# Kernel optimization log

Measured on AMD Instinct MI355X. Metric: run time of the kernel, lower is better.

Reference implementation:

```python
import jax, jax.numpy as jnp
import numpy as np

HEADS = 8
HIDDEN = 512
SEQ = 1024
BATCH = 8
SCALE = 1.2
TOPK = round(0.05 * SEQ)  # 51, as in mode='stocastic'


def setup_inputs() -> dict:
    key = jax.random.key(0)
    ks = jax.random.split(key, 12)
    d = HIDDEN
    s = 0.02
    return {
        "Query_x": jax.random.normal(ks[0], (BATCH, SEQ, d), jnp.float32),
        "KeyandValue_x": jax.random.normal(ks[1], (BATCH, SEQ, d), jnp.float32),
        "Wq": jax.random.normal(ks[2], (d, d), jnp.float32) * s,
        "bq": jnp.zeros((d,), jnp.float32),
        "Wk": jax.random.normal(ks[3], (d, d), jnp.float32) * s,
        "bk": jnp.zeros((d,), jnp.float32),
        "Wv": jax.random.normal(ks[4], (d, d), jnp.float32) * s,
        "bv": jnp.zeros((d,), jnp.float32),
        "Wo": jax.random.normal(ks[5], (d, d), jnp.float32) * s,
        "bo": jnp.zeros((d,), jnp.float32),
        "randidx": jax.random.randint(ks[6], (round(0.1 * SEQ),), 0, SEQ, jnp.int32),
    }


def _split_heads(x, B, S):
    # torch: split last dim into heads chunks, cat along dim 0 -> [heads*B, S, dk]
    dk = HIDDEN // HEADS
    return x.reshape(B, S, HEADS, dk).transpose(2, 0, 1, 3).reshape(HEADS * B, S, dk)


def _merge_heads(x, B, S):
    dk = HIDDEN // HEADS
    return x.reshape(HEADS, B, S, dk).transpose(1, 2, 0, 3).reshape(B, S, HIDDEN)


def moderate_attention(a, randidx):
    # a: [N, S, L] softmaxed attention. Scale top-k + random columns by SCALE,
    # then renormalize rows. torch scatter_ writes a*SCALE gathered from the
    # pre-scatter tensor, so duplicate indices are idempotent -> boolean mask.
    N, S, L = a.shape
    _, idx = jax.lax.top_k(a, TOPK)                       # [N, S, k]
    rand_b = jnp.broadcast_to(randidx.astype(idx.dtype), (N, S, randidx.shape[0]))
    all_idx = jnp.concatenate([idx, rand_b], axis=-1)      # [N, S, k+r]
    n_ix = jnp.arange(N)[:, None, None]
    q_ix = jnp.arange(S)[None, :, None]
    sel = jnp.zeros(a.shape, bool).at[n_ix, q_ix, all_idx].set(True)
    a2 = jnp.where(sel, a * SCALE, a)
    return a2 / jnp.sum(a2, axis=-1, keepdims=True)


def reference(Query_x, KeyandValue_x, Wq, bq, Wk, bk, Wv, bv, Wo, bo, randidx):
    B, S, _ = Query_x.shape
    dk = HIDDEN // HEADS
    Q = _split_heads(Query_x @ Wq + bq, B, S)          # [H*B, S, dk]
    K = _split_heads(KeyandValue_x @ Wk + bk, B, S)
    V = _split_heads(KeyandValue_x @ Wv + bv, B, S)
    scores = jnp.einsum('nqd,nkd->nqk', Q, K) / jnp.sqrt(jnp.float32(dk))
    a = jax.nn.softmax(scores, axis=-1)
    a = moderate_attention(a, randidx)
    out = jnp.einsum('nqk,nkd->nqd', a, V)
    return _merge_heads(out, B, S) @ Wo + bo
```

## Files before the change

kernel.cpp:

```cpp
#include <hip/hip_runtime.h>
#include <stdint.h>

typedef unsigned short ushort_t;
typedef __bf16 bf16x8 __attribute__((ext_vector_type(8)));
typedef _Float16 f16x8v __attribute__((ext_vector_type(8)));
typedef __fp16 fp16x2 __attribute__((ext_vector_type(2)));
typedef float f32x4 __attribute__((ext_vector_type(4)));

#define SEQ   1024
#define DK    64
#define TOPK_N 51
#define RSCALE 1.2f
#define LOG2E    1.44269504089f
#define LOG2_12  0.26303440583f

#define OFF_WT  0
#define OFF_Q   (4*512*512)
#define OFF_K   (OFF_Q  + 64*1024*64)
#define OFF_V   (OFF_K  + 64*1024*64)
#define OFF_QX  (OFF_V  + 64*1024*64)
#define OFF_KVX (OFF_QX + 8192*512)
#define OFF_MASK (OFF_KVX + 8192*512)
#define OFF_A   OFF_QX

static __device__ __forceinline__ ushort_t f2bf(float f){
  union { float f; unsigned u; } x; x.f = f;
  unsigned r = x.u + 0x7FFFu + ((x.u >> 16) & 1u);
  return (ushort_t)(r >> 16);
}
static __device__ __forceinline__ ushort_t f2h(float f){
  union { _Float16 h; ushort_t u; } x; x.h = (_Float16)f; return x.u;
}
static __device__ __forceinline__ float h2f(ushort_t u){
  union { ushort_t u; _Float16 h; } x; x.u = u; return (float)x.h;
}
static __device__ __forceinline__ unsigned pk2(float a, float b){
  union { fp16x2 h; unsigned u; } x;
  x.h = __builtin_amdgcn_cvt_pkrtz(a, b);
  return x.u;
}
static __device__ __forceinline__ unsigned pkrne(float a, float b){
  return (unsigned)f2h(a) | ((unsigned)f2h(b) << 16);
}
static __device__ __forceinline__ bf16x8 frag16(const ushort_t* p){
  union { uint4 u; bf16x8 b; } x; x.u = *(const uint4*)p; return x.b;
}
static __device__ __forceinline__ f16x8v frag16h(const ushort_t* p){
  union { uint4 u; f16x8v h; } x; x.u = *(const uint4*)p; return x.h;
}
static __device__ __forceinline__ void gll16(const ushort_t* g, ushort_t* lds){
  __builtin_amdgcn_global_load_lds((const __attribute__((address_space(1))) unsigned*)g,
                                   (__attribute__((address_space(3))) unsigned*)lds,
                                   16, 0, 0);
}

__global__ __launch_bounds__(256) void prep_k(const float* qx, const float* kvx,
    const float* Wq, const float* Wk, const float* Wv, const float* Wo,
    const int* ridx, int nrand, ushort_t* ws){
  __shared__ ushort_t t[64][72];
  __shared__ unsigned wds[64];
  int bid = blockIdx.x, tid = threadIdx.x;

  if (bid < 4096){
    const float* src = (bid >= 2048) ? kvx : qx;
    ushort_t* dst = ws + ((bid >= 2048) ? OFF_KVX : OFF_QX);
    int i = ((bid & 2047)*256 + tid) * 8;
    float4 a = *(const float4*)(src + i);
    float4 b = *(const float4*)(src + i + 4);
    union { ushort_t s[8]; uint4 u; } p;
    p.s[0]=f2bf(a.x); p.s[1]=f2bf(a.y); p.s[2]=f2bf(a.z); p.s[3]=f2bf(a.w);
    p.s[4]=f2bf(b.x); p.s[5]=f2bf(b.y); p.s[6]=f2bf(b.z); p.s[7]=f2bf(b.w);
    *(uint4*)(dst + i) = p.u;
  } else if (bid < 4352){
    int rb = bid - 4096;
    int z = rb >> 6, rem = rb & 63;
    const float* W = z==0?Wq: z==1?Wk: z==2?Wv: Wo;
    ushort_t* O = ws + OFF_WT + (size_t)z*512*512;
    int kt = (rem >> 3)*64, nt = (rem & 7)*64;
    int r0 = tid>>3, c8 = (tid&7)*8;
    #pragma unroll
    for (int p=0;p<2;p++){
      int r = p*32 + r0;
      float4 a = *(const float4*)&W[(size_t)(kt+r)*512 + nt + c8];
      float4 b = *(const float4*)&W[(size_t)(kt+r)*512 + nt + c8 + 4];
      t[r][c8+0]=f2bf(a.x); t[r][c8+1]=f2bf(a.y); t[r][c8+2]=f2bf(a.z); t[r][c8+3]=f2bf(a.w);
      t[r][c8+4]=f2bf(b.x); t[r][c8+5]=f2bf(b.y); t[r][c8+6]=f2bf(b.z); t[r][c8+7]=f2bf(b.w);
    }
    __syncthreads();
    #pragma unroll
    for (int p=0;p<2;p++){
      int r = p*32 + r0;
      union { ushort_t s[8]; uint4 u; } tmp;
      #pragma unroll
      for (int j=0;j<8;j++) tmp.s[j] = t[c8+j][r];
      *(uint4*)&O[(size_t)(nt+r)*512 + kt + c8] = tmp.u;
    }
  } else {
    if (tid < 64) wds[tid] = 0;
    __syncthreads();
    for (int i = tid; i < nrand; i += 256){
      int col = ridx[i];
      atomicOr(&wds[(col >> 3) & 63], 1u << (((col >> 9) << 3) | (col & 7)));
    }
    __syncthreads();
    if (tid < 64) (ws + OFF_MASK)[tid] = (ushort_t)wds[tid];
  }
}

__global__ __launch_bounds__(256, 3) void gemm_k(ushort_t* ws, const float* bq, const float* bk,
    const float* bv, const float* bo, float* dout, int base_mode){
  int mode = base_mode + blockIdx.z;
  const ushort_t* X  = (mode==0)? ws+OFF_QX : (mode==3)? ws+OFF_A : ws+OFF_KVX;
  const ushort_t* WT = ws + OFF_WT + (size_t)mode*(512*512);
  const float* bias  = (mode==0)?bq:(mode==1)?bk:(mode==2)?bv:bo;
  ushort_t* out = (mode==0)? ws+OFF_Q : (mode==1)? ws+OFF_K : ws+OFF_V;

  __shared__ ushort_t sA[3][128*32];
  __shared__ ushort_t sB[3][128*32];
  int tid = threadIdx.x, lane = tid & 63, w = tid >> 6;
  int wm = w & 1, wn = w >> 1;
  int m0 = blockIdx.y * 128, n0 = blockIdx.x * 128;
  int r16 = lane & 15, quad = lane >> 4;
  int srow = tid >> 2, sch = tid & 3;

  const f32x4 zero = {0.f,0.f,0.f,0.f};
  f32x4 acc[4][4];
  #pragma unroll
  for (int i=0;i<4;i++)
    #pragma unroll
    for (int j=0;j<4;j++) acc[i][j] = zero;

  #define STAGE(t, buf)                                                        \
    {                                                                          \
      int k0 = (t)*32;                                                         \
      _Pragma("unroll")                                                        \
      for (int p=0;p<2;p++){                                                   \
        int row = p*64 + srow;                                                 \
        int gch = sch ^ ((row >> 1) & 3);                                      \
        gll16(X  + (size_t)(m0+row)*512 + k0 + gch*8, &sA[buf][(p*64 + (w<<4))*32]); \
        gll16(WT + (size_t)(n0+row)*512 + k0 + gch*8, &sB[buf][(p*64 + (w<<4))*32]); \
      }                                                                        \
    }

  STAGE(0, 0);
  STAGE(1, 1);

  #pragma unroll
  for (int t = 0; t < 16; t++){
    if (t < 15) asm volatile("s_waitcnt vmcnt(4)" ::: "memory");
    else        asm volatile("s_waitcnt vmcnt(0)" ::: "memory");
    __builtin_amdgcn_s_barrier();
    asm volatile("" ::: "memory");
    if (t < 14) STAGE(t+2, (t+2)%3);
    int buf = t % 3;
    bf16x8 aF[4], bF[4];
    #pragma unroll
    for (int i=0;i<4;i++){
      int row = wm*64 + i*16 + r16;
      aF[i] = frag16(&sA[buf][row*32 + ((quad ^ ((row >> 1) & 3))*8)]);
    }
    #pragma unroll
    for (int j=0;j<4;j++){
      int row = wn*64 + j*16 + r16;
      bF[j] = frag16(&sB[buf][row*32 + ((quad ^ ((row >> 1) & 3))*8)]);
    }
    __builtin_amdgcn_s_setprio(1);
    #pragma unroll
    for (int i=0;i<4;i++)
      #pragma unroll
      for (int j=0;j<4;j++)
        acc[i][j] = __builtin_amdgcn_mfma_f32_16x16x32_bf16(aF[i], bF[j], acc[i][j], 0,0,0);
    __builtin_amdgcn_s_setprio(0);
  }
  #undef STAGE

  #pragma unroll
  for (int i=0;i<4;i++){
    int rowbase = m0 + wm*64 + i*16 + quad*4;
    #pragma unroll
    for (int j=0;j<4;j++){
      int col = n0 + wn*64 + j*16 + r16;
      float bsv = bias[col];
      if (mode == 3){
        #pragma unroll
        for (int r=0;r<4;r++)
          dout[(size_t)(rowbase+r)*512 + col] = acc[i][j][r] + bsv;
      } else if (mode == 2){
        int b = rowbase >> 10, s = rowbase & 1023;
        int h = col >> 6, d = col & 63;
        int nh = h*8 + b;
        union { ushort_t sh[4]; uint2 u2; } pk;
        #pragma unroll
        for (int r=0;r<4;r++) pk.sh[r] = f2h(acc[i][j][r] + bsv);
        *(uint2*)&out[ (((size_t)nh*128 + (s>>3))*64 + d)*8 + (s&4) ] = pk.u2;
      } else if (mode == 1){
        int b = rowbase >> 10;
        int h = col >> 6, d = col & 63;
        int nh = h*8 + b;
        size_t base = (size_t)nh*65536 + (size_t)(d>>3)*8192 + (d&7);
        #pragma unroll
        for (int r=0;r<4;r++){
          int s = (rowbase + r) & 1023;
          out[ base + (size_t)s*8 ] = f2bf(acc[i][j][r] + bsv);
        }
      } else {
        int h = col >> 6, d = col & 63;
        #pragma unroll
        for (int r=0;r<4;r++){
          int row = rowbase + r;
          int b = row >> 10, s = row & 1023;
          int nh = h*8 + b;
          out[ ((size_t)nh*1024 + s)*64 + d ] = f2bf((acc[i][j][r] + bsv)*0.125f);
        }
      }
    }
  }
}

__global__ __launch_bounds__(256, 4) void attn_k(const ushort_t* ws_q, const ushort_t* ws_k,
     const ushort_t* ws_v, const ushort_t* maskp, ushort_t* attn){
  __shared__ __align__(16) ushort_t sS[16*1024];

  int tid = threadIdx.x, lane = tid&63, w = tid>>6;
  int r16 = lane&15, quad = lane>>4;
  int gid = blockIdx.x;
  int n  = (gid & 7)*8 + ((gid >> 3) >> 6);
  int q0 = ((gid >> 3) & 63) * 16;
  const ushort_t* Qn = ws_q + (size_t)n*SEQ*DK;
  const ushort_t* Kn = ws_k + (size_t)n*SEQ*DK;
  const ushort_t* Vb = ws_v + (size_t)n*SEQ*DK;

  unsigned rmask = (unsigned)maskp[lane];

  bf16x8 aQ[2];
  #pragma unroll
  for (int t=0;t<2;t++)
    aQ[t] = frag16(Qn + (size_t)(q0 + r16)*64 + t*32 + quad*8);

  const f32x4 zero = {0.f,0.f,0.f,0.f};

  #pragma unroll
  for (int half=0; half<2; half++){
    f32x4 acc[8];
    #pragma unroll
    for (int i=0;i<8;i++) acc[i] = zero;
    #pragma unroll
    for (int grp=0; grp<2; grp++){
      int c = half*2 + grp;
      bf16x8 bF[8];
      #pragma unroll
      for (int u=0;u<4;u++){
        int key = c*256 + w*64 + u*16 + r16;
        bF[u*2+0] = frag16(Kn + ((size_t)(quad    )*1024 + key)*8);
        bF[u*2+1] = frag16(Kn + ((size_t)(4 + quad)*1024 + key)*8);
      }
      __builtin_amdgcn_s_setprio(1);
      #pragma unroll
      for (int u=0;u<4;u++){
        int t8 = grp*4 + u;
        acc[t8] = __builtin_amdgcn_mfma_f32_16x16x32_bf16(bF[u*2+0], aQ[0], acc[t8], 0,0,0);
        acc[t8] = __builtin_amdgcn_mfma_f32_16x16x32_bf16(bF[u*2+1], aQ[1], acc[t8], 0,0,0);
      }
      __builtin_amdgcn_s_setprio(0);
    }
    int rs = r16 & 7;
    #pragma unroll
    for (int grp=0; grp<2; grp++)
      #pragma unroll
      for (int u=0;u<4;u++){
        int kb = (half*2+grp)*256 + w*64 + u*16 + quad*4;
        f32x4 a = acc[grp*4+u];
        uint2 o;
        o.x = pkrne(a[0], a[1]);
        o.y = pkrne(a[2], a[3]);
        *(uint2*)(sS + r16*1024 + (((kb>>3) ^ rs) << 3) + (kb & 4)) = o;
      }
  }
  __syncthreads();

  float v[4][16];
  float vmax[4];
  #pragma unroll
  for (int r=0;r<4;r++){
    int row = w*4 + r, rs = row & 7;
    const ushort_t* bp = sS + row*1024 + ((lane ^ rs) * 8);
    uint4 lo4 = *(const uint4*)bp;
    uint4 hi4 = *(const uint4*)(bp + 512);
    unsigned wl[8] = {lo4.x, lo4.y, lo4.z, lo4.w, hi4.x, hi4.y, hi4.z, hi4.w};
    float m = -3.0e38f;
    #pragma unroll
    for (int k=0;k<8;k++){
      float a = h2f((ushort_t)(wl[k] & 0xffffu));
      float b = h2f((ushort_t)(wl[k] >> 16));
      v[r][2*k] = a; v[r][2*k+1] = b;
      m = fmaxf(m, fmaxf(a, b));
    }
    vmax[r] = m;
  }
  #pragma unroll
  for (int r=0;r<4;r++)
    #pragma unroll
    for (int j=0;j<16;j++)
      asm volatile("" : "+v"(v[r][j]));

  #pragma unroll
  for (int off=32; off>=1; off>>=1)
    #pragma unroll
    for (int r=0;r<4;r++) vmax[r] = fmaxf(vmax[r], __shfl_xor(vmax[r], off));

  float blo[4], bhi[4];
  #pragma unroll
  for (int r=0;r<4;r++){ bhi[r] = vmax[r]; blo[r] = vmax[r] - 1.0f; }
  #pragma unroll 1
  for (int it=0; it<9; it++){
    #pragma unroll
    for (int r=0;r<4;r++){
      float mid = 0.5f*(blo[r]+bhi[r]);
      int cnt = 0;
      #pragma unroll
      for (int j=0;j<16;j++)
        cnt += __popcll(__ballot(v[r][j] >= mid));
      bool ge = (cnt >= TOPK_N);
      blo[r] = ge ? mid : blo[r];
      bhi[r] = ge ? bhi[r] : mid;
    }
  }
  float fb[16];
  #pragma unroll
  for (int j=0;j<16;j++) fb[j] = ((rmask >> j) & 1u) ? LOG2_12 : 0.0f;
  float sC = LOG2_12;
  asm volatile("" : "+v"(sC));

  float ls[4];
  #pragma unroll
  for (int r=0;r<4;r++){
    float thr = blo[r], s = 0.f;
    #pragma unroll
    for (int j=0;j<16;j++){
      float tb = (v[r][j] >= thr) ? sC : fb[j];
      float e = __builtin_amdgcn_exp2f(
                  __builtin_fmaf(v[r][j] - vmax[r], LOG2E, tb));
      v[r][j] = e; s += e;
    }
    ls[r] = s;
  }
  #pragma unroll
  for (int off=32; off>=1; off>>=1)
    #pragma unroll
    for (int r=0;r<4;r++) ls[r] += __shfl_xor(ls[r], off);
  #pragma unroll
  for (int r=0;r<4;r++){
    int row = w*4 + r, rs = row & 7;
    float rinv = 1.0f / ls[r];
    ushort_t* bp = sS + row*1024 + ((lane ^ rs) * 8);
    uint4 o0, o1;
    o0.x = pk2(v[r][0]*rinv,  v[r][1]*rinv);
    o0.y = pk2(v[r][2]*rinv,  v[r][3]*rinv);
    o0.z = pk2(v[r][4]*rinv,  v[r][5]*rinv);
    o0.w = pk2(v[r][6]*rinv,  v[r][7]*rinv);
    o1.x = pk2(v[r][8]*rinv,  v[r][9]*rinv);
    o1.y = pk2(v[r][10]*rinv, v[r][11]*rinv);
    o1.z = pk2(v[r][12]*rinv, v[r][13]*rinv);
    o1.w = pk2(v[r][14]*rinv, v[r][15]*rinv);
    *(uint4*)bp = o0;
    *(uint4*)(bp + 512) = o1;
  }
  __syncthreads();

  f32x4 oa0 = zero, oa1 = zero;
  int dd = w*16 + r16;
  #pragma unroll
  for (int kb2=0; kb2<8; kb2++){
    f16x8v bV[4], aP[4];
    #pragma unroll
    for (int u=0;u<4;u++){
      int g8 = (kb2*4 + u)*4 + quad;
      bV[u] = frag16h(Vb + ((size_t)g8*64 + dd)*8);
      aP[u] = frag16h(sS + r16*1024 + ((g8 ^ (r16&7))*8));
    }
    __builtin_amdgcn_s_setprio(1);
    #pragma unroll
    for (int u=0;u<4;u++){
      if (u&1) oa1 = __builtin_amdgcn_mfma_f32_16x16x32_f16(aP[u], bV[u], oa1, 0,0,0);
      else     oa0 = __builtin_amdgcn_mfma_f32_16x16x32_f16(aP[u], bV[u], oa0, 0,0,0);
    }
    __builtin_amdgcn_s_setprio(0);
  }
  f32x4 oacc = oa0 + oa1;

  int h = n >> 3, b = n & 7;
  #pragma unroll
  for (int r=0;r<4;r++){
    int s = q0 + quad*4 + r;
    attn[ ((size_t)(b*1024 + s))*512 + h*64 + w*16 + r16 ] = f2bf(oacc[r]);
  }
}

extern "C" void kernel_launch(void* const* d_in, const int* in_sizes, int n_in,
                              void* d_out, int out_size, void* d_ws, size_t ws_size,
                              hipStream_t stream){
  const float* Qx  = (const float*)d_in[0];
  const float* KVx = (const float*)d_in[1];
  const float* Wq  = (const float*)d_in[2];
  const float* bq  = (const float*)d_in[3];
  const float* Wk  = (const float*)d_in[4];
  const float* bk  = (const float*)d_in[5];
  const float* Wv  = (const float*)d_in[6];
  const float* bv  = (const float*)d_in[7];
  const float* Wo  = (const float*)d_in[8];
  const float* bo  = (const float*)d_in[9];
  const int* ridx  = (const int*)d_in[10];
  int nrand = in_sizes[10];
  ushort_t* ws = (ushort_t*)d_ws;
  float* dout = (float*)d_out;

  prep_k<<<4353, 256, 0, stream>>>(Qx, KVx, Wq, Wk, Wv, Wo, ridx, nrand, ws);
  gemm_k<<<dim3(4,64,3), 256, 0, stream>>>(ws, bq, bk, bv, bo, dout, 0);
  attn_k<<<4096, 256, 0, stream>>>(ws+OFF_Q, ws+OFF_K, ws+OFF_V, ws+OFF_MASK, ws+OFF_A);
  gemm_k<<<dim3(4,64,1), 256, 0, stream>>>(ws, bq, bk, bv, bo, dout, 3);
}
```

Measured before the change: 217.1 us.

## Fuse fp32-to-bf16 input conversion into QKV projection GEMM A-tile loads

Removes the separate prep pass that converted Query_x and KeyandValue_x to bf16 in workspace. The QKV GEMM now loads fp32 activations into registers one k-step ahead, converts them to bf16 and writes them into a double-buffered swizzled LDS tile. The weight tile keeps its async global-to-LDS path. This avoids a full read-write round trip of 32 MB of inputs, but the A-operand path becomes synchronous register staging, reads twice the bytes per GEMM tile, and repeats the conversion across the four N-blocks.

```diff
diff --git a/kernel.cpp b/kernel.cpp
--- a/kernel.cpp
+++ b/kernel.cpp
@@ -18,10 +18,8 @@
 #define OFF_Q   (4*512*512)
 #define OFF_K   (OFF_Q  + 64*1024*64)
 #define OFF_V   (OFF_K  + 64*1024*64)
-#define OFF_QX  (OFF_V  + 64*1024*64)
-#define OFF_KVX (OFF_QX + 8192*512)
-#define OFF_MASK (OFF_KVX + 8192*512)
-#define OFF_A   OFF_QX
+#define OFF_A   (OFF_V  + 64*1024*64)
+#define OFF_MASK (OFF_A + 8192*512)
 
 static __device__ __forceinline__ ushort_t f2bf(float f){
   union { float f; unsigned u; } x; x.f = f;
@@ -54,25 +52,15 @@
                                    16, 0, 0);
 }
 
-__global__ __launch_bounds__(256) void prep_k(const float* qx, const float* kvx,
+__global__ __launch_bounds__(256) void prep_k(
     const float* Wq, const float* Wk, const float* Wv, const float* Wo,
     const int* ridx, int nrand, ushort_t* ws){
   __shared__ ushort_t t[64][72];
   __shared__ unsigned wds[64];
   int bid = blockIdx.x, tid = threadIdx.x;
 
-  if (bid < 4096){
-    const float* src = (bid >= 2048) ? kvx : qx;
-    ushort_t* dst = ws + ((bid >= 2048) ? OFF_KVX : OFF_QX);
-    int i = ((bid & 2047)*256 + tid) * 8;
-    float4 a = *(const float4*)(src + i);
-    float4 b = *(const float4*)(src + i + 4);
-    union { ushort_t s[8]; uint4 u; } p;
-    p.s[0]=f2bf(a.x); p.s[1]=f2bf(a.y); p.s[2]=f2bf(a.z); p.s[3]=f2bf(a.w);
-    p.s[4]=f2bf(b.x); p.s[5]=f2bf(b.y); p.s[6]=f2bf(b.z); p.s[7]=f2bf(b.w);
-    *(uint4*)(dst + i) = p.u;
-  } else if (bid < 4352){
-    int rb = bid - 4096;
+  if (bid < 256){
+    int rb = bid;
     int z = rb >> 6, rem = rb & 63;
     const float* W = z==0?Wq: z==1?Wk: z==2?Wv: Wo;
     ushort_t* O = ws + OFF_WT + (size_t)z*512*512;
@@ -107,10 +95,13 @@
   }
 }
 
-__global__ __launch_bounds__(256, 3) void gemm_k(ushort_t* ws, const float* bq, const float* bk,
-    const float* bv, const float* bo, float* dout, int base_mode){
+__global__ __launch_bounds__(256, 3) void gemm_k(ushort_t* ws,
+    const float* qx, const float* kvx,
+    const float* bq, const float* bk, const float* bv, const float* bo,
+    float* dout, int base_mode){
   int mode = base_mode + blockIdx.z;
-  const ushort_t* X  = (mode==0)? ws+OFF_QX : (mode==3)? ws+OFF_A : ws+OFF_KVX;
+  const float*    Xf = (mode==0)? qx : kvx;
+  const ushort_t* Xb = ws + OFF_A;
   const ushort_t* WT = ws + OFF_WT + (size_t)mode*(512*512);
   const float* bias  = (mode==0)?bq:(mode==1)?bk:(mode==2)?bv:bo;
   ushort_t* out = (mode==0)? ws+OFF_Q : (mode==1)? ws+OFF_K : ws+OFF_V;
@@ -122,6 +113,7 @@
   int m0 = blockIdx.y * 128, n0 = blockIdx.x * 128;
   int r16 = lane & 15, quad = lane >> 4;
   int srow = tid >> 2, sch = tid & 3;
+  int arow = tid >> 1, acp = (tid & 1) * 2;
 
   const f32x4 zero = {0.f,0.f,0.f,0.f};
   f32x4 acc[4][4];
@@ -130,49 +122,124 @@
     #pragma unroll
     for (int j=0;j<4;j++) acc[i][j] = zero;
 
-  #define STAGE(t, buf)                                                        \
+  #define STAGE_B(t, buf)                                                      \
     {                                                                          \
       int k0 = (t)*32;                                                         \
       _Pragma("unroll")                                                        \
       for (int p=0;p<2;p++){                                                   \
         int row = p*64 + srow;                                                 \
         int gch = sch ^ ((row >> 1) & 3);                                      \
-        gll16(X  + (size_t)(m0+row)*512 + k0 + gch*8, &sA[buf][(p*64 + (w<<4))*32]); \
         gll16(WT + (size_t)(n0+row)*512 + k0 + gch*8, &sB[buf][(p*64 + (w<<4))*32]); \
       }                                                                        \
     }
-
-  STAGE(0, 0);
-  STAGE(1, 1);
-
-  #pragma unroll
-  for (int t = 0; t < 16; t++){
-    if (t < 15) asm volatile("s_waitcnt vmcnt(4)" ::: "memory");
-    else        asm volatile("s_waitcnt vmcnt(0)" ::: "memory");
-    __builtin_amdgcn_s_barrier();
-    asm volatile("" ::: "memory");
-    if (t < 14) STAGE(t+2, (t+2)%3);
-    int buf = t % 3;
-    bf16x8 aF[4], bF[4];
-    #pragma unroll
-    for (int i=0;i<4;i++){
-      int row = wm*64 + i*16 + r16;
-      aF[i] = frag16(&sA[buf][row*32 + ((quad ^ ((row >> 1) & 3))*8)]);
-    }
-    #pragma unroll
-    for (int j=0;j<4;j++){
-      int row = wn*64 + j*16 + r16;
-      bF[j] = frag16(&sB[buf][row*32 + ((quad ^ ((row >> 1) & 3))*8)]);
-    }
-    __builtin_amdgcn_s_setprio(1);
-    #pragma unroll
-    for (int i=0;i<4;i++)
-      #pragma unroll
-      for (int j=0;j<4;j++)
-        acc[i][j] = __builtin_amdgcn_mfma_f32_16x16x32_bf16(aF[i], bF[j], acc[i][j], 0,0,0);
-    __builtin_amdgcn_s_setprio(0);
-  }
-  #undef STAGE
+  #define STAGE_A3(t, buf)                                                     \
+    {                                                                          \
+      int k0 = (t)*32;                                                         \
+      _Pragma("unroll")                                                        \
+      for (int p=0;p<2;p++){                                                   \
+        int row = p*64 + srow;                                                 \
+        int gch = sch ^ ((row >> 1) & 3);                                      \
+        gll16(Xb + (size_t)(m0+row)*512 + k0 + gch*8, &sA[buf][(p*64 + (w<<4))*32]); \
+      }                                                                        \
+    }
+  #define AISSUE(t, rg)                                                        \
+    {                                                                          \
+      int k0 = (t)*32;                                                         \
+      _Pragma("unroll")                                                        \
+      for (int c=0;c<2;c++){                                                   \
+        int lc = (acp + c) ^ ((arow >> 1) & 3);                                \
+        const float* sp = Xf + (size_t)(m0+arow)*512 + k0 + lc*8;              \
+        rg[c*2+0] = *(const float4*)sp;                                        \
+        rg[c*2+1] = *(const float4*)(sp + 4);                                  \
+      }                                                                        \
+    }
+  #define AWRITE(buf, rg)                                                      \
+    {                                                                          \
+      _Pragma("unroll")                                                        \
+      for (int c=0;c<2;c++){                                                   \
+        union { ushort_t s[8]; uint4 u; } pkk;                                 \
+        pkk.s[0]=f2bf(rg[c*2+0].x); pkk.s[1]=f2bf(rg[c*2+0].y);                \
+        pkk.s[2]=f2bf(rg[c*2+0].z); pkk.s[3]=f2bf(rg[c*2+0].w);                \
+        pkk.s[4]=f2bf(rg[c*2+1].x); pkk.s[5]=f2bf(rg[c*2+1].y);                \
+        pkk.s[6]=f2bf(rg[c*2+1].z); pkk.s[7]=f2bf(rg[c*2+1].w);                \
+        *(uint4*)&sA[buf][arow*32 + (acp + c)*8] = pkk.u;                      \
+      }                                                                        \
+    }
+
+  if (base_mode == 3){
+    STAGE_A3(0, 0); STAGE_B(0, 0);
+    STAGE_A3(1, 1); STAGE_B(1, 1);
+    #pragma unroll
+    for (int t = 0; t < 16; t++){
+      if (t < 15) asm volatile("s_waitcnt vmcnt(4)" ::: "memory");
+      else        asm volatile("s_waitcnt vmcnt(0)" ::: "memory");
+      __builtin_amdgcn_s_barrier();
+      asm volatile("" ::: "memory");
+      if (t < 14){ STAGE_A3(t+2, (t+2)%3); STAGE_B(t+2, (t+2)%3); }
+      int buf = t % 3;
+      bf16x8 aF[4], bF[4];
+      #pragma unroll
+      for (int i=0;i<4;i++){
+        int row = wm*64 + i*16 + r16;
+        aF[i] = frag16(&sA[buf][row*32 + ((quad ^ ((row >> 1) & 3))*8)]);
+      }
+      #pragma unroll
+      for (int j=0;j<4;j++){
+        int row = wn*64 + j*16 + r16;
+        bF[j] = frag16(&sB[buf][row*32 + ((quad ^ ((row >> 1) & 3))*8)]);
+      }
+      __builtin_amdgcn_s_setprio(1);
+      #pragma unroll
+      for (int i=0;i<4;i++)
+        #pragma unroll
+        for (int j=0;j<4;j++)
+          acc[i][j] = __builtin_amdgcn_mfma_f32_16x16x32_bf16(aF[i], bF[j], acc[i][j], 0,0,0);
+      __builtin_amdgcn_s_setprio(0);
+    }
+  } else {
+    float4 rg[4];
+    AISSUE(0, rg); STAGE_B(0, 0);
+    for (int t = 0; t < 16; t++){
+      float4 rn[4];
+      if (t < 15){
+        AISSUE(t+1, rn);
+        STAGE_B(t+1, (t+1)%3);
+        asm volatile("s_waitcnt vmcnt(6)" ::: "memory");
+      } else {
+        asm volatile("s_waitcnt vmcnt(0)" ::: "memory");
+      }
+      int abuf = t & 1;
+      AWRITE(abuf, rg);
+      asm volatile("s_waitcnt lgkmcnt(0)" ::: "memory");
+      __builtin_amdgcn_s_barrier();
+      asm volatile("" ::: "memory");
+      int bbuf = t % 3;
+      bf16x8 aF[4], bF[4];
+      #pragma unroll
+      for (int i=0;i<4;i++){
+        int row = wm*64 + i*16 + r16;
+        aF[i] = frag16(&sA[abuf][row*32 + ((quad ^ ((row >> 1) & 3))*8)]);
+      }
+      #pragma unroll
+      for (int j=0;j<4;j++){
+        int row = wn*64 + j*16 + r16;
+        bF[j] = frag16(&sB[bbuf][row*32 + ((quad ^ ((row >> 1) & 3))*8)]);
+      }
+      __builtin_amdgcn_s_setprio(1);
+      #pragma unroll
+      for (int i=0;i<4;i++)
+        #pragma unroll
+        for (int j=0;j<4;j++)
+          acc[i][j] = __builtin_amdgcn_mfma_f32_16x16x32_bf16(aF[i], bF[j], acc[i][j], 0,0,0);
+      __builtin_amdgcn_s_setprio(0);
+      #pragma unroll
+      for (int c=0;c<4;c++) rg[c] = rn[c];
+    }
+  }
+  #undef STAGE_B
+  #undef STAGE_A3
+  #undef AISSUE
+  #undef AWRITE
 
   #pragma unroll
   for (int i=0;i<4;i++){
@@ -414,8 +481,8 @@
   ushort_t* ws = (ushort_t*)d_ws;
   float* dout = (float*)d_out;
 
-  prep_k<<<4353, 256, 0, stream>>>(Qx, KVx, Wq, Wk, Wv, Wo, ridx, nrand, ws);
-  gemm_k<<<dim3(4,64,3), 256, 0, stream>>>(ws, bq, bk, bv, bo, dout, 0);
+  prep_k<<<257, 256, 0, stream>>>(Wq, Wk, Wv, Wo, ridx, nrand, ws);
+  gemm_k<<<dim3(4,64,3), 256, 0, stream>>>(ws, Qx, KVx, bq, bk, bv, bo, dout, 0);
   attn_k<<<4096, 256, 0, stream>>>(ws+OFF_Q, ws+OFF_K, ws+OFF_V, ws+OFF_MASK, ws+OFF_A);
-  gemm_k<<<dim3(4,64,1), 256, 0, stream>>>(ws, bq, bk, bv, bo, dout, 3);
-}
+  gemm_k<<<dim3(4,64,1), 256, 0, stream>>>(ws, Qx, KVx, bq, bk, bv, bo, dout, 3);
+}
```

Measured after the change: 221.1 us. Within noise of the previous version (+1.8%).
